# Performance work log

Measured on AMD Instinct MI355X. Metric: run time of the kernel, lower is better.

Reference implementation:

```python
import math
import jax, jax.numpy as jnp
import numpy as np

D_MODEL = 1024
N_HEADS = 16
BLOCK = 2048
EPS2 = 0.0487        # sparse_eps2 / BOOTSTRAP_EPS2
ROPE_BASE = 10000.0


def _riemann_zeros(K):
    """Approximate imaginary parts of the first K nontrivial zeta zeros by
    Newton-inverting t/(2pi)*log(t/(2pi*e)) = n - 7/8 (standard asymptotic).
    Note: gamma is normalized by gamma[0] in the module, so only the relative
    spacing matters for the math."""
    n = np.arange(1, K + 1, dtype=np.float64)
    t = 10.0 + 6.0 * n  # safe init, > 2*pi
    for _ in range(60):
        f = t / (2 * np.pi) * np.log(t / (2 * np.pi * np.e)) - (n - 0.875)
        fp = np.log(t / (2 * np.pi)) / (2 * np.pi)
        t = t - f / fp
    return t


def _constants(N, K):
    g = _riemann_zeros(K)
    g = g / g[0]
    denom = 0.25 + g * g
    w_re = (0.5 / denom).astype(np.float32)          # [K]
    w_im = (-g / denom).astype(np.float32)           # [K]
    pos = np.arange(N, dtype=np.float32)
    k_idx = np.arange(K, dtype=np.float32)
    inv_freq = ROPE_BASE ** (-k_idx / K)
    phase = pos[:, None] * inv_freq[None, :]          # [N,K]
    cos_p = np.cos(phase).astype(np.float32)
    sin_p = np.sin(phase).astype(np.float32)
    log1p = np.log1p(pos)
    log_decay = (0.5 * (log1p[None, :] - log1p[:, None])).astype(np.float32)  # [N,N]
    tril = np.tril(np.ones((N, N), dtype=bool))
    return (jnp.asarray(w_re), jnp.asarray(w_im), jnp.asarray(cos_p),
            jnp.asarray(sin_p), jnp.asarray(log_decay), jnp.asarray(tril))


def setup_inputs() -> dict:
    key = jax.random.key(0)
    kx, kq, kk, kv, ko = jax.random.split(key, 5)
    B, N, D = 2, BLOCK, D_MODEL
    s = 0.02
    return {
        "x": jax.random.normal(kx, (B, N, D), jnp.float32),
        "Wq": jax.random.normal(kq, (D, D), jnp.float32) * s,
        "Wk": jax.random.normal(kk, (D, D), jnp.float32) * s,
        "Wv": jax.random.normal(kv, (D, D), jnp.float32) * s,
        "Wo": jax.random.normal(ko, (D, D), jnp.float32) * s,
    }


def reference(x, Wq, Wk, Wv, Wo):
    B, N, D = x.shape
    H = N_HEADS
    dh = D // H
    K = dh // 2
    w_re, w_im, cos_p, sin_p, log_decay, tril = _constants(N, K)

    q = (x @ Wq).reshape(B, N, H, dh)
    k = (x @ Wk).reshape(B, N, H, dh)
    v = (x @ Wv).reshape(B, N, H, dh)

    q_re, q_im = q[..., 0::2], q[..., 1::2]           # [B,N,H,K]
    k_re, k_im = k[..., 0::2], k[..., 1::2]

    cos_b = cos_p[None, :, None, :]                   # [1,N,1,K]
    sin_b = sin_p[None, :, None, :]
    # RoPE rotation in complex form
    qt_re = cos_b * q_re + sin_b * q_im
    qt_im = cos_b * q_im - sin_b * q_re
    kt_re = cos_b * k_re + sin_b * k_im
    kt_im = cos_b * k_im - sin_b * k_re

    wr = w_re[None, None, None, :]
    wi = w_im[None, None, None, :]
    # zeta-amplitude complex weighting of q
    qh_re = wr * qt_re - wi * qt_im
    qh_im = wr * qt_im + wi * qt_re

    # Re(sum_k w_k * q~_i conj(k~_j)) via two real GEMMs
    scores = (jnp.einsum('bihk,bjhk->bhij', qh_re, kt_re)
              + jnp.einsum('bihk,bjhk->bhij', qh_im, kt_im)) / math.sqrt(dh)

    # decay_mode == 'mult'
    scores = scores * jnp.exp(log_decay)[None, None, :, :]

    scores = jnp.where(tril[None, None, :, :], scores, -jnp.inf)
    attn = jax.nn.softmax(scores, axis=-1)

    # bootstrap_sparse: keep top-k per row, renormalize
    kk = max(1, math.ceil(EPS2 * N))
    if kk < N:
        vals, _ = jax.lax.top_k(attn, kk)
        thresh = vals[..., -1:]
        mask = (attn >= thresh).astype(attn.dtype)
        masked = attn * mask
        attn = masked / jnp.maximum(masked.sum(-1, keepdims=True), 1e-9)

    out = jnp.einsum('bhij,bjhd->bihd', attn, v).reshape(B, N, D)
    return out @ Wo
```

## Files before the change

kernel.cpp:

```cpp
#include <hip/hip_runtime.h>
#include <math.h>

#define B_SZ 2
#define N_SEQ 2048
#define DM 1024
#define H_HEADS 16
#define DH 64
#define KC 32
#define TOPK 100
#define TQ 16
#define KT 128
#define NTMAX 16
#define FCAP 192
#define CSTRIDE 132

typedef _Float16 half2_t __attribute__((ext_vector_type(2)));
typedef _Float16 half4_t __attribute__((ext_vector_type(4)));
typedef _Float16 half8_t __attribute__((ext_vector_type(8)));
typedef float floatx4 __attribute__((ext_vector_type(4)));
typedef unsigned short ushort4_t __attribute__((ext_vector_type(4)));

__device__ __forceinline__ unsigned short h2us(_Float16 h) {
  unsigned short u; __builtin_memcpy(&u, &h, 2); return u;
}
__device__ __forceinline__ _Float16 us2h(unsigned short u) {
  _Float16 h; __builtin_memcpy(&h, &u, 2); return h;
}
__device__ __forceinline__ unsigned okey16(unsigned short us) {
  return (us & 0x8000u) ? (unsigned)(unsigned short)~us
                        : (unsigned)(us | 0x8000u);
}

__device__ __forceinline__ void stage16(const _Float16* g, _Float16* lds_base,
                                        int lane) {
#if __has_builtin(__builtin_amdgcn_global_load_lds)
  __builtin_amdgcn_global_load_lds(
      (const __attribute__((address_space(1))) void*)g,
      (__attribute__((address_space(3))) void*)lds_base, 16, 0, 0);
#else
  *(half8_t*)(lds_base + lane * 8) = *(const half8_t*)g;
#endif
}

__global__ void const_kernel(float* __restrict__ wre, float* __restrict__ wim) {
  __shared__ double g0s;
  const int k = threadIdx.x;
  const double PI = 3.14159265358979323846;
  const double E_ = 2.71828182845904523536;
  double n = (double)(k + 1);
  double t = 10.0 + 6.0 * n;
  for (int it = 0; it < 16; ++it) {
    double f  = t / (2.0 * PI) * log(t / (2.0 * PI * E_)) - (n - 0.875);
    double fp = log(t / (2.0 * PI)) / (2.0 * PI);
    t = t - f / fp;
  }
  if (k == 0) g0s = t;
  __syncthreads();
  double g = t / g0s;
  double denom = 0.25 + g * g;
  wre[k] = (float)(0.5 / denom);
  wim[k] = (float)(-g / denom);
}

__global__ __launch_bounds__(256) void rope_kernel(float* __restrict__ cosT,
                                                   float* __restrict__ sinT) {
  int idx = blockIdx.x * 256 + threadIdx.x;
  int kk = idx & 31, n = idx >> 5;
  float f = -(float)kk * (13.2877123795494f / 32.0f);
  float inv_freq = exp2f(f);
  float ph = (float)n * inv_freq;
  cosT[idx] = cosf(ph);
  sinT[idx] = sinf(ph);
}

__global__ __launch_bounds__(256) void cast_x(const float* __restrict__ x,
                                              _Float16* __restrict__ xh) {
  int idx = blockIdx.x * 256 + threadIdx.x;
  float4 v = ((const float4*)x)[idx];
  half4_t h;
  h[0] = (_Float16)v.x; h[1] = (_Float16)v.y;
  h[2] = (_Float16)v.z; h[3] = (_Float16)v.w;
  ((half4_t*)xh)[idx] = h;
}

__global__ __launch_bounds__(256) void transpose_cast(
    const float* __restrict__ W0, const float* __restrict__ W1,
    const float* __restrict__ W2, const float* __restrict__ W3,
    _Float16* __restrict__ T0, _Float16* __restrict__ T1,
    _Float16* __restrict__ T2, _Float16* __restrict__ T3) {
  __shared__ float t[64][65];
  const float* W; _Float16* T;
  switch (blockIdx.z) {
    case 0: W = W0; T = T0; break;
    case 1: W = W1; T = T1; break;
    case 2: W = W2; T = T2; break;
    default: W = W3; T = T3; break;
  }
  const int bx = blockIdx.x;
  const int by = blockIdx.y;
  const int tid = threadIdx.x;
  const int c = tid & 15, rr = tid >> 4;
#pragma unroll
  for (int i = 0; i < 4; ++i) {
    int k = rr + i * 16;
    float4 v = *(const float4*)(W + (size_t)(bx * 64 + k) * DM + by * 64 + c * 4);
    t[k][c * 4 + 0] = v.x; t[k][c * 4 + 1] = v.y;
    t[k][c * 4 + 2] = v.z; t[k][c * 4 + 3] = v.w;
  }
  __syncthreads();
#pragma unroll
  for (int i = 0; i < 4; ++i) {
    int n = rr + i * 16;
    half4_t h;
    h[0] = (_Float16)t[c * 4 + 0][n];
    h[1] = (_Float16)t[c * 4 + 1][n];
    h[2] = (_Float16)t[c * 4 + 2][n];
    h[3] = (_Float16)t[c * 4 + 3][n];
    *(half4_t*)(T + (size_t)(by * 64 + n) * DM + bx * 64 + c * 4) = h;
  }
}

__device__ __forceinline__ void gemm_loop(const _Float16* __restrict__ A,
                                          const _Float16* __restrict__ Bt,
                                          _Float16* As, _Float16* Bs,
                                          floatx4 (&acc)[4][4]) {
  const int tid = threadIdx.x;
  const int wave = tid >> 6, lane = tid & 63;
  const int wm = wave >> 1, wn = wave & 1;
  const int bm = blockIdx.x * 128, bn = blockIdx.y * 128;
  const int grow = lane >> 3;
  const int gch  = (lane & 7) ^ grow;
  const int l16 = lane & 15, lq = lane >> 4;
  const int sw  = l16 & 7;

  for (int k0 = 0; k0 < DM; k0 += 64) {
    __syncthreads();
#pragma unroll
    for (int s = 0; s < 4; ++s) {
      const int seg = wave * 4 + s;
      stage16(A + (size_t)(bm + seg * 8 + grow) * DM + k0 + gch * 8,
              As + seg * 512, lane);
      stage16(Bt + (size_t)(bn + seg * 8 + grow) * DM + k0 + gch * 8,
              Bs + seg * 512, lane);
    }
    __syncthreads();
    half8_t af[2][4], bf[2][4];
#pragma unroll
    for (int kk2 = 0; kk2 < 2; ++kk2) {
#pragma unroll
      for (int mi = 0; mi < 4; ++mi)
        af[kk2][mi] = *(const half8_t*)(As + (wm * 64 + mi * 16 + l16) * 64 +
                                        ((kk2 * 4 + lq) ^ sw) * 8);
#pragma unroll
      for (int ni = 0; ni < 4; ++ni)
        bf[kk2][ni] = *(const half8_t*)(Bs + (wn * 64 + ni * 16 + l16) * 64 +
                                        ((kk2 * 4 + lq) ^ sw) * 8);
    }
#pragma unroll
    for (int kk2 = 0; kk2 < 2; ++kk2)
#pragma unroll
      for (int mi = 0; mi < 4; ++mi)
#pragma unroll
        for (int ni = 0; ni < 4; ++ni)
          acc[mi][ni] = __builtin_amdgcn_mfma_f32_16x16x32_f16(
              af[kk2][mi], bf[kk2][ni], acc[mi][ni], 0, 0, 0);
  }
}

__global__ __launch_bounds__(256) void gemm_qkv_fused(
    const _Float16* __restrict__ xh, const _Float16* __restrict__ Wt0,
    const _Float16* __restrict__ Wt1, const _Float16* __restrict__ Wt2,
    const float* __restrict__ wre, const float* __restrict__ wim,
    const float* __restrict__ cosT, const float* __restrict__ sinT,
    float* __restrict__ qhO, _Float16* __restrict__ kthO,
    _Float16* __restrict__ vthO) {
  __shared__ __align__(16) _Float16 smem[2 * 128 * 64];
  _Float16* As = smem;
  _Float16* Bs = smem + 128 * 64;
  const int z = blockIdx.z;
  const _Float16* Bt = (z == 0) ? Wt0 : (z == 1) ? Wt1 : Wt2;
  floatx4 acc[4][4] = {};
  gemm_loop(xh, Bt, As, Bs, acc);
  __syncthreads();

  float* cbuf = (float*)smem;
  const int tid = threadIdx.x;
  const int wave = tid >> 6, lane = tid & 63;
  const int wm = wave >> 1, wn = wave & 1;
  const int bm = blockIdx.x * 128, bn = blockIdx.y * 128;
  const int l16 = lane & 15, lq = lane >> 4;

  const int h2 = tid >> 7, t7 = tid & 127;
  const int rl = t7 >> 2, q4 = t7 & 3;
  const int hh = (bn >> 6) + h2;
  const int row_nom = bm + (rl >> 4) * 64 + (rl & 15);
  const int kk0 = q4 * 8;

#pragma unroll
  for (int mi = 0; mi < 4; ++mi) {
#pragma unroll
    for (int ni = 0; ni < 4; ++ni)
#pragma unroll
      for (int r = 0; r < 4; ++r)
        cbuf[(wm * 16 + lq * 4 + r) * CSTRIDE + wn * 64 + ni * 16 + l16] =
            acc[mi][ni][r];
    __syncthreads();

    const int row = row_nom + mi * 16;
    const int b = row >> 11, n = row & (N_SEQ - 1);
    const float* crow = cbuf + rl * CSTRIDE + h2 * 64;
    const size_t base = ((size_t)((b * H_HEADS + hh) * N_SEQ + n)) * DH;

    if (z == 2) {
      const int d0 = q4 * 16;
      half8_t o0, o1;
#pragma unroll
      for (int j = 0; j < 8; ++j) {
        o0[j] = (_Float16)crow[d0 + j];
        o1[j] = (_Float16)crow[d0 + 8 + j];
      }
      *(half8_t*)(vthO + base + d0) = o0;
      *(half8_t*)(vthO + base + d0 + 8) = o1;
    } else if (z == 1) {
      const float sj = 0.125f * sqrtf(1.0f + (float)n);
      half8_t ore, oim;
#pragma unroll
      for (int j = 0; j < 8; ++j) {
        const int kk = kk0 + j;
        const float re = crow[2 * kk], im = crow[2 * kk + 1];
        const float cp = cosT[n * 32 + kk], sp = sinT[n * 32 + kk];
        ore[j] = (_Float16)((cp * re + sp * im) * sj);
        oim[j] = (_Float16)((cp * im - sp * re) * sj);
      }
      *(half8_t*)(kthO + base + kk0) = ore;
      *(half8_t*)(kthO + base + 32 + kk0) = oim;
    } else {
      float ore[8], oim[8];
#pragma unroll
      for (int j = 0; j < 8; ++j) {
        const int kk = kk0 + j;
        const float re = crow[2 * kk], im = crow[2 * kk + 1];
        const float cp = cosT[n * 32 + kk], sp = sinT[n * 32 + kk];
        const float t_re = cp * re + sp * im;
        const float t_im = cp * im - sp * re;
        const float wr = wre[kk], wi = wim[kk];
        ore[j] = wr * t_re - wi * t_im;
        oim[j] = wr * t_im + wi * t_re;
      }
      float4 v0 = {ore[0], ore[1], ore[2], ore[3]};
      float4 v1 = {ore[4], ore[5], ore[6], ore[7]};
      float4 v2 = {oim[0], oim[1], oim[2], oim[3]};
      float4 v3 = {oim[4], oim[5], oim[6], oim[7]};
      *(float4*)(qhO + base + kk0) = v0;
      *(float4*)(qhO + base + kk0 + 4) = v1;
      *(float4*)(qhO + base + 32 + kk0) = v2;
      *(float4*)(qhO + base + 32 + kk0 + 4) = v3;
    }
    if (mi < 3) __syncthreads();
  }
}

__global__ __launch_bounds__(256) void gemm_out_mfma(
    const _Float16* __restrict__ A, const _Float16* __restrict__ Bt,
    float* __restrict__ C) {
  __shared__ _Float16 As[128 * 64];
  __shared__ _Float16 Bs[128 * 64];
  floatx4 acc[4][4] = {};
  gemm_loop(A, Bt, As, Bs, acc);
  const int tid = threadIdx.x;
  const int wave = tid >> 6, lane = tid & 63;
  const int wm = wave >> 1, wn = wave & 1;
  const int bm = blockIdx.x * 128, bn = blockIdx.y * 128;
  const int l16 = lane & 15, lq = lane >> 4;
#pragma unroll
  for (int mi = 0; mi < 4; ++mi)
#pragma unroll
    for (int ni = 0; ni < 4; ++ni) {
      const int col = bn + wn * 64 + ni * 16 + l16;
#pragma unroll
      for (int r = 0; r < 4; ++r) {
        const int row = bm + wm * 64 + mi * 16 + lq * 4 + r;
        C[(size_t)row * DM + col] = acc[mi][ni][r];
      }
    }
}

__global__ __launch_bounds__(512, 4) void attn_kernel(
    const float* __restrict__ qh, const _Float16* __restrict__ kth,
    const _Float16* __restrict__ vth, _Float16* __restrict__ oh) {
  __shared__ unsigned hist[TQ][128];
  __shared__ unsigned final_[TQ][FCAP];
  __shared__ float mredw[8][TQ];
  __shared__ float rowm[TQ], rowsum[TQ];
  __shared__ unsigned cnt2[TQ], tkA[TQ];
  __shared__ int sh_b[TQ], sh_k[TQ];

  const int tile = gridDim.x - 1 - blockIdx.x;
  const int bh   = blockIdx.y;
  const int i0   = tile * TQ;
  const int tid  = threadIdx.x;
  const int wv = tid >> 6, lane = tid & 63;
  const int l16 = lane & 15, lq = lane >> 4;
  const int jbase = wv * 16 + l16;

  const _Float16* kbase = kth + (size_t)bh * N_SEQ * DH;
  const _Float16* vbase = vth + (size_t)bh * N_SEQ * DH;
  const _Float16* kfrag = kbase + (size_t)jbase * DH + lq * 8;

#pragma unroll
  for (int u = 0; u < 4; ++u) ((unsigned*)hist)[u * 512 + tid] = 0;
  if (tid < TQ) { cnt2[tid] = 0; rowsum[tid] = 0.f; }

  half8_t af0, af1;
  {
    const float* qrow = qh + ((size_t)(bh * N_SEQ + i0 + l16)) * DH;
    const float rs = rsqrtf(1.0f + (float)(i0 + l16));
    float4 a0 = *(const float4*)(qrow + lq * 8);
    float4 a1 = *(const float4*)(qrow + lq * 8 + 4);
    float4 b0 = *(const float4*)(qrow + 32 + lq * 8);
    float4 b1 = *(const float4*)(qrow + 32 + lq * 8 + 4);
    af0[0] = (_Float16)(a0.x * rs); af0[1] = (_Float16)(a0.y * rs);
    af0[2] = (_Float16)(a0.z * rs); af0[3] = (_Float16)(a0.w * rs);
    af0[4] = (_Float16)(a1.x * rs); af0[5] = (_Float16)(a1.y * rs);
    af0[6] = (_Float16)(a1.z * rs); af0[7] = (_Float16)(a1.w * rs);
    af1[0] = (_Float16)(b0.x * rs); af1[1] = (_Float16)(b0.y * rs);
    af1[2] = (_Float16)(b0.z * rs); af1[3] = (_Float16)(b0.w * rs);
    af1[4] = (_Float16)(b1.x * rs); af1[5] = (_Float16)(b1.y * rs);
    af1[6] = (_Float16)(b1.z * rs); af1[7] = (_Float16)(b1.w * rs);
  }

  const int ntile = (i0 + TQ + KT - 1) / KT;

  ushort4_t scr[NTMAX];
  float mx[4] = {-INFINITY, -INFINITY, -INFINITY, -INFINITY};

  __syncthreads();

#pragma unroll
  for (int t = 0; t < NTMAX; ++t) {
    if (t < ntile) {
      const _Float16* kp = kfrag + (size_t)t * KT * DH;
      half8_t bf0 = *(const half8_t*)kp;
      half8_t bf1 = *(const half8_t*)(kp + 32);
      floatx4 acc = {};
      acc = __builtin_amdgcn_mfma_f32_16x16x32_f16(af0, bf0, acc, 0, 0, 0);
      acc = __builtin_amdgcn_mfma_f32_16x16x32_f16(af1, bf1, acc, 0, 0, 0);
      const int jc = t * KT + jbase;
      ushort4_t s4;
#pragma unroll
      for (int r = 0; r < 4; ++r) {
        float sc = acc[r];
        s4[r] = h2us((_Float16)sc);
        if (jc <= i0 + lq * 4 + r) {
          mx[r] = fmaxf(mx[r], sc);
          unsigned hb = okey16(s4[r]) >> 8;
          atomicAdd(&hist[lq * 4 + r][hb >> 1], 1u << ((hb & 1) * 16));
        }
      }
      scr[t] = s4;
    }
  }

#pragma unroll
  for (int g = 1; g <= 8; g <<= 1)
#pragma unroll
    for (int r = 0; r < 4; ++r) mx[r] = fmaxf(mx[r], __shfl_xor(mx[r], g));
  if (l16 == 0)
#pragma unroll
    for (int r = 0; r < 4; ++r) mredw[wv][lq * 4 + r] = mx[r];
  __syncthreads();
  if (tid < TQ) {
    float m = mredw[0][tid];
#pragma unroll
    for (int w = 1; w < 8; ++w) m = fmaxf(m, mredw[w][tid]);
    rowm[tid] = m;
  }

  const int srow = tid >> 5, ts = tid & 31;
  {
    const int L = i0 + srow + 1;
    if (L > TOPK) {
      const unsigned* hrow = hist[srow];
      const int base_u = 124 - 4 * ts;
      unsigned h0 = hrow[base_u + 0], h1 = hrow[base_u + 1];
      unsigned h2 = hrow[base_u + 2], h3 = hrow[base_u + 3];
      int c[8] = {(int)(h3 >> 16), (int)(h3 & 0xffffu),
                  (int)(h2 >> 16), (int)(h2 & 0xffffu),
                  (int)(h1 >> 16), (int)(h1 & 0xffffu),
                  (int)(h0 >> 16), (int)(h0 & 0xffffu)};
      int ssum = 0;
#pragma unroll
      for (int k2 = 0; k2 < 8; ++k2) ssum += c[k2];
      int inc = ssum;
#pragma unroll
      for (int d = 1; d < 32; d <<= 1) {
        int o = __shfl_up(inc, d, 32);
        if (ts >= d) inc += o;
      }
      const int excl = inc - ssum;
      if (excl < TOPK && TOPK <= inc) {
        int cum = excl, k2 = 0;
#pragma unroll
        for (; k2 < 8; ++k2) {
          if (cum + c[k2] >= TOPK) break;
          cum += c[k2];
        }
        sh_b[srow] = 255 - 8 * ts - k2;
        sh_k[srow] = TOPK - cum;
      }
    } else if (ts == 0) {
      sh_b[srow] = 256;
      sh_k[srow] = 0;
      tkA[srow] = 0;
    }
  }
  __syncthreads();
#pragma unroll
  for (int u = 0; u < 4; ++u) ((unsigned*)hist)[u * 512 + tid] = 0;
  int bh4[4];
#pragma unroll
  for (int r = 0; r < 4; ++r) bh4[r] = sh_b[lq * 4 + r];
  __syncthreads();

#pragma unroll
  for (int t = 0; t < NTMAX; ++t) {
    if (t < ntile) {
      const int jc = t * KT + jbase;
      ushort4_t s4 = scr[t];
#pragma unroll
      for (int r = 0; r < 4; ++r) {
        if (jc <= i0 + lq * 4 + r) {
          unsigned key = okey16(s4[r]);
          if ((int)(key >> 8) == bh4[r]) {
            unsigned lb = key & 255u;
            atomicAdd(&hist[lq * 4 + r][lb >> 1], 1u << ((lb & 1) * 16));
          }
        }
      }
    }
  }
  __syncthreads();

  {
    const int L = i0 + srow + 1;
    if (L > TOPK) {
      const int krem = sh_k[srow];
      const unsigned* hrow = hist[srow];
      const int base_u = 124 - 4 * ts;
      unsigned h0 = hrow[base_u + 0], h1 = hrow[base_u + 1];
      unsigned h2 = hrow[base_u + 2], h3 = hrow[base_u + 3];
      int c[8] = {(int)(h3 >> 16), (int)(h3 & 0xffffu),
                  (int)(h2 >> 16), (int)(h2 & 0xffffu),
                  (int)(h1 >> 16), (int)(h1 & 0xffffu),
                  (int)(h0 >> 16), (int)(h0 & 0xffffu)};
      int ssum = 0;
#pragma unroll
      for (int k2 = 0; k2 < 8; ++k2) ssum += c[k2];
      int inc = ssum;
#pragma unroll
      for (int d = 1; d < 32; d <<= 1) {
        int o = __shfl_up(inc, d, 32);
        if (ts >= d) inc += o;
      }
      const int excl = inc - ssum;
      if (excl < krem && krem <= inc) {
        int cum = excl, k2 = 0;
#pragma unroll
        for (; k2 < 8; ++k2) {
          if (cum + c[k2] >= krem) break;
          cum += c[k2];
        }
        tkA[srow] = ((unsigned)sh_b[srow] << 8) | (unsigned)(255 - 8 * ts - k2);
      }
    }
  }
  __syncthreads();

  unsigned tk4[4]; float m4[4];
#pragma unroll
  for (int r = 0; r < 4; ++r) {
    tk4[r] = tkA[lq * 4 + r];
    m4[r]  = rowm[lq * 4 + r];
  }
  float lsum[4] = {0.f, 0.f, 0.f, 0.f};
#pragma unroll
  for (int t = 0; t < NTMAX; ++t) {
    if (t < ntile) {
      const int jc = t * KT + jbase;
      ushort4_t s4 = scr[t];
#pragma unroll
      for (int r = 0; r < 4; ++r) {
        if (jc <= i0 + lq * 4 + r) {
          unsigned short us = s4[r];
          if (okey16(us) >= tk4[r]) {
            float p = __expf((float)us2h(us) - m4[r]);
            lsum[r] += p;
            unsigned pos = atomicAdd(&cnt2[lq * 4 + r], 1u);
            if (pos < FCAP)
              final_[lq * 4 + r][pos] =
                  ((unsigned)h2us((_Float16)p) << 16) | (unsigned)jc;
          }
        }
      }
    }
  }
#pragma unroll
  for (int g = 1; g <= 8; g <<= 1)
#pragma unroll
    for (int r = 0; r < 4; ++r) lsum[r] += __shfl_xor(lsum[r], g);
  if (l16 == 0)
#pragma unroll
    for (int r = 0; r < 4; ++r) atomicAdd(&rowsum[lq * 4 + r], lsum[r]);
  __syncthreads();

  for (int rr = wv; rr < TQ; rr += 8) {
    const int nfin = (int)min(cnt2[rr], (unsigned)FCAP);
    const float inv = 1.0f / rowsum[rr];
    float acc = 0.f;
#pragma unroll 4
    for (int s = 0; s < nfin; ++s) {
      unsigned e = final_[rr][s];
      const int jj = (int)(e & 0xffffu);
      const float p = (float)us2h((unsigned short)(e >> 16));
      acc += p * (float)vbase[(size_t)jj * DH + lane];
    }
    const int b = bh >> 4, h = bh & 15;
    const int i = i0 + rr;
    oh[((size_t)(b * N_SEQ + i)) * DM + h * DH + lane] = (_Float16)(acc * inv);
  }
}

extern "C" void kernel_launch(void* const* d_in, const int* in_sizes, int n_in,
                              void* d_out, int out_size, void* d_ws, size_t ws_size,
                              hipStream_t stream) {
  const float* x  = (const float*)d_in[0];
  const float* Wq = (const float*)d_in[1];
  const float* Wk = (const float*)d_in[2];
  const float* Wv = (const float*)d_in[3];
  const float* Wo = (const float*)d_in[4];
  float* out = (float*)d_out;
  char* ws = (char*)d_ws;

  const size_t MAT = (size_t)B_SZ * N_SEQ * DM;
  const size_t WSZ = (size_t)DM * DM;

  float*    qh   = (float*)ws;                       ws += MAT * 4;
  _Float16* xh   = (_Float16*)ws;                    ws += MAT * 2;
  _Float16* kth  = (_Float16*)ws;                    ws += MAT * 2;
  _Float16* vth  = (_Float16*)ws;                    ws += MAT * 2;
  _Float16* Wt0  = (_Float16*)ws;                    ws += WSZ * 2;
  _Float16* Wt1  = (_Float16*)ws;                    ws += WSZ * 2;
  _Float16* Wt2  = (_Float16*)ws;                    ws += WSZ * 2;
  _Float16* Wt3  = (_Float16*)ws;                    ws += WSZ * 2;
  float*    wre  = (float*)ws;                       ws += KC * 4;
  float*    wim  = (float*)ws;                       ws += KC * 4;
  float*    cosT = (float*)ws;                       ws += (size_t)N_SEQ * KC * 4;
  float*    sinT = (float*)ws;                       ws += (size_t)N_SEQ * KC * 4;
  _Float16* oh   = xh;

  const_kernel<<<1, 32, 0, stream>>>(wre, wim);
  rope_kernel<<<(N_SEQ * KC) / 256, 256, 0, stream>>>(cosT, sinT);
  cast_x<<<(int)(MAT / 4 / 256), 256, 0, stream>>>(x, xh);
  transpose_cast<<<dim3(16, 16, 4), 256, 0, stream>>>(Wq, Wk, Wv, Wo,
                                                      Wt0, Wt1, Wt2, Wt3);
  gemm_qkv_fused<<<dim3(32, 8, 3), 256, 0, stream>>>(
      xh, Wt0, Wt1, Wt2, wre, wim, cosT, sinT, qh, kth, vth);
  attn_kernel<<<dim3(N_SEQ / TQ, B_SZ * H_HEADS), 512, 0, stream>>>(
      qh, kth, vth, oh);
  gemm_out_mfma<<<dim3(32, 8, 1), 256, 0, stream>>>(oh, Wt3, out);
}
```

Before: 391.1 us.

## Merge setup kernels, add XCD-aware GEMM tile mapping, interleave two-row PV gather

```diff
diff --git a/kernel.cpp b/kernel.cpp
--- a/kernel.cpp
+++ b/kernel.cpp
@@ -42,45 +42,50 @@
 #endif
 }
 
-__global__ void const_kernel(float* __restrict__ wre, float* __restrict__ wim) {
-  __shared__ double g0s;
-  const int k = threadIdx.x;
-  const double PI = 3.14159265358979323846;
-  const double E_ = 2.71828182845904523536;
-  double n = (double)(k + 1);
-  double t = 10.0 + 6.0 * n;
-  for (int it = 0; it < 16; ++it) {
-    double f  = t / (2.0 * PI) * log(t / (2.0 * PI * E_)) - (n - 0.875);
-    double fp = log(t / (2.0 * PI)) / (2.0 * PI);
-    t = t - f / fp;
-  }
-  if (k == 0) g0s = t;
-  __syncthreads();
-  double g = t / g0s;
-  double denom = 0.25 + g * g;
-  wre[k] = (float)(0.5 / denom);
-  wim[k] = (float)(-g / denom);
-}
-
-__global__ __launch_bounds__(256) void rope_kernel(float* __restrict__ cosT,
-                                                   float* __restrict__ sinT) {
-  int idx = blockIdx.x * 256 + threadIdx.x;
-  int kk = idx & 31, n = idx >> 5;
-  float f = -(float)kk * (13.2877123795494f / 32.0f);
-  float inv_freq = exp2f(f);
-  float ph = (float)n * inv_freq;
-  cosT[idx] = cosf(ph);
-  sinT[idx] = sinf(ph);
-}
-
-__global__ __launch_bounds__(256) void cast_x(const float* __restrict__ x,
-                                              _Float16* __restrict__ xh) {
-  int idx = blockIdx.x * 256 + threadIdx.x;
-  float4 v = ((const float4*)x)[idx];
-  half4_t h;
-  h[0] = (_Float16)v.x; h[1] = (_Float16)v.y;
-  h[2] = (_Float16)v.z; h[3] = (_Float16)v.w;
-  ((half4_t*)xh)[idx] = h;
+__global__ __launch_bounds__(256) void setup_kernel(
+    const float* __restrict__ x, _Float16* __restrict__ xh,
+    float* __restrict__ cosT, float* __restrict__ sinT,
+    float* __restrict__ wre, float* __restrict__ wim) {
+  const int bi = blockIdx.x;
+  if (bi < 4096) {
+    int idx = bi * 256 + threadIdx.x;
+    float4 v = ((const float4*)x)[idx];
+    half4_t h;
+    h[0] = (_Float16)v.x; h[1] = (_Float16)v.y;
+    h[2] = (_Float16)v.z; h[3] = (_Float16)v.w;
+    ((half4_t*)xh)[idx] = h;
+  } else if (bi < 4096 + 256) {
+    int idx = (bi - 4096) * 256 + threadIdx.x;
+    int kk = idx & 31, n = idx >> 5;
+    float f = -(float)kk * (13.2877123795494f / 32.0f);
+    float inv_freq = exp2f(f);
+    float ph = (float)n * inv_freq;
+    cosT[idx] = cosf(ph);
+    sinT[idx] = sinf(ph);
+  } else {
+    __shared__ double g0s;
+    const int k = threadIdx.x;
+    const double PI = 3.14159265358979323846;
+    const double E_ = 2.71828182845904523536;
+    double t = 0.0;
+    if (k < 32) {
+      double n = (double)(k + 1);
+      t = 10.0 + 6.0 * n;
+      for (int it = 0; it < 16; ++it) {
+        double f  = t / (2.0 * PI) * log(t / (2.0 * PI * E_)) - (n - 0.875);
+        double fp = log(t / (2.0 * PI)) / (2.0 * PI);
+        t = t - f / fp;
+      }
+      if (k == 0) g0s = t;
+    }
+    __syncthreads();
+    if (k < 32) {
+      double g = t / g0s;
+      double denom = 0.25 + g * g;
+      wre[k] = (float)(0.5 / denom);
+      wim[k] = (float)(-g / denom);
+    }
+  }
 }
 
 __global__ __launch_bounds__(256) void transpose_cast(
@@ -123,11 +128,11 @@
 __device__ __forceinline__ void gemm_loop(const _Float16* __restrict__ A,
                                           const _Float16* __restrict__ Bt,
                                           _Float16* As, _Float16* Bs,
+                                          int bm, int bn,
                                           floatx4 (&acc)[4][4]) {
   const int tid = threadIdx.x;
   const int wave = tid >> 6, lane = tid & 63;
   const int wm = wave >> 1, wn = wave & 1;
-  const int bm = blockIdx.x * 128, bn = blockIdx.y * 128;
   const int grow = lane >> 3;
   const int gch  = (lane & 7) ^ grow;
   const int l16 = lane & 15, lq = lane >> 4;
@@ -165,6 +170,12 @@
           acc[mi][ni] = __builtin_amdgcn_mfma_f32_16x16x32_f16(
               af[kk2][mi], bf[kk2][ni], acc[mi][ni], 0, 0, 0);
   }
+}
+
+__device__ __forceinline__ void xcd_decode(int flat, int& bm, int& bn) {
+  const int o = (flat & 7) * 32 + (flat >> 3);
+  bm = (o >> 3) * 128;
+  bn = (o & 7) * 128;
 }
 
 __global__ __launch_bounds__(256) void gemm_qkv_fused(
@@ -179,15 +190,16 @@
   _Float16* Bs = smem + 128 * 64;
   const int z = blockIdx.z;
   const _Float16* Bt = (z == 0) ? Wt0 : (z == 1) ? Wt1 : Wt2;
+  int bm, bn;
+  xcd_decode(blockIdx.x, bm, bn);
   floatx4 acc[4][4] = {};
-  gemm_loop(xh, Bt, As, Bs, acc);
+  gemm_loop(xh, Bt, As, Bs, bm, bn, acc);
   __syncthreads();
 
   float* cbuf = (float*)smem;
   const int tid = threadIdx.x;
   const int wave = tid >> 6, lane = tid & 63;
   const int wm = wave >> 1, wn = wave & 1;
-  const int bm = blockIdx.x * 128, bn = blockIdx.y * 128;
   const int l16 = lane & 15, lq = lane >> 4;
 
   const int h2 = tid >> 7, t7 = tid & 127;
@@ -265,12 +277,13 @@
     float* __restrict__ C) {
   __shared__ _Float16 As[128 * 64];
   __shared__ _Float16 Bs[128 * 64];
+  int bm, bn;
+  xcd_decode(blockIdx.x, bm, bn);
   floatx4 acc[4][4] = {};
-  gemm_loop(A, Bt, As, Bs, acc);
+  gemm_loop(A, Bt, As, Bs, bm, bn, acc);
   const int tid = threadIdx.x;
   const int wave = tid >> 6, lane = tid & 63;
   const int wm = wave >> 1, wn = wave & 1;
-  const int bm = blockIdx.x * 128, bn = blockIdx.y * 128;
   const int l16 = lane & 15, lq = lane >> 4;
 #pragma unroll
   for (int mi = 0; mi < 4; ++mi)
@@ -513,20 +526,32 @@
     for (int r = 0; r < 4; ++r) atomicAdd(&rowsum[lq * 4 + r], lsum[r]);
   __syncthreads();
 
-  for (int rr = wv; rr < TQ; rr += 8) {
-    const int nfin = (int)min(cnt2[rr], (unsigned)FCAP);
-    const float inv = 1.0f / rowsum[rr];
-    float acc = 0.f;
-#pragma unroll 4
-    for (int s = 0; s < nfin; ++s) {
-      unsigned e = final_[rr][s];
-      const int jj = (int)(e & 0xffffu);
-      const float p = (float)us2h((unsigned short)(e >> 16));
-      acc += p * (float)vbase[(size_t)jj * DH + lane];
+  {
+    const int r0 = wv, r1 = wv + 8;
+    const int n0 = (int)min(cnt2[r0], (unsigned)FCAP);
+    const int n1 = (int)min(cnt2[r1], (unsigned)FCAP);
+    const float inv0 = 1.0f / rowsum[r0];
+    const float inv1 = 1.0f / rowsum[r1];
+    float a0 = 0.f, a1 = 0.f;
+    const int nmx = n0 > n1 ? n0 : n1;
+#pragma unroll 8
+    for (int s = 0; s < nmx; ++s) {
+      if (s < n0) {
+        unsigned e = final_[r0][s];
+        a0 += (float)us2h((unsigned short)(e >> 16)) *
+              (float)vbase[(size_t)(e & 0xffffu) * DH + lane];
+      }
+      if (s < n1) {
+        unsigned e = final_[r1][s];
+        a1 += (float)us2h((unsigned short)(e >> 16)) *
+              (float)vbase[(size_t)(e & 0xffffu) * DH + lane];
+      }
     }
     const int b = bh >> 4, h = bh & 15;
-    const int i = i0 + rr;
-    oh[((size_t)(b * N_SEQ + i)) * DM + h * DH + lane] = (_Float16)(acc * inv);
+    oh[((size_t)(b * N_SEQ + i0 + r0)) * DM + h * DH + lane] =
+        (_Float16)(a0 * inv0);
+    oh[((size_t)(b * N_SEQ + i0 + r1)) * DM + h * DH + lane] =
+        (_Float16)(a1 * inv1);
   }
 }
 
@@ -558,14 +583,12 @@
   float*    sinT = (float*)ws;                       ws += (size_t)N_SEQ * KC * 4;
   _Float16* oh   = xh;
 
-  const_kernel<<<1, 32, 0, stream>>>(wre, wim);
-  rope_kernel<<<(N_SEQ * KC) / 256, 256, 0, stream>>>(cosT, sinT);
-  cast_x<<<(int)(MAT / 4 / 256), 256, 0, stream>>>(x, xh);
+  setup_kernel<<<4096 + 256 + 1, 256, 0, stream>>>(x, xh, cosT, sinT, wre, wim);
   transpose_cast<<<dim3(16, 16, 4), 256, 0, stream>>>(Wq, Wk, Wv, Wo,
                                                       Wt0, Wt1, Wt2, Wt3);
-  gemm_qkv_fused<<<dim3(32, 8, 3), 256, 0, stream>>>(
+  gemm_qkv_fused<<<dim3(256, 1, 3), 256, 0, stream>>>(
       xh, Wt0, Wt1, Wt2, wre, wim, cosT, sinT, qh, kth, vth);
   attn_kernel<<<dim3(N_SEQ / TQ, B_SZ * H_HEADS), 512, 0, stream>>>(
       qh, kth, vth, oh);
-  gemm_out_mfma<<<dim3(32, 8, 1), 256, 0, stream>>>(oh, Wt3, out);
-}
+  gemm_out_mfma<<<dim3(256), 256, 0, stream>>>(oh, Wt3, out);
+}
```

Result: slower. 563.7 us (+44.2%).
